# Performance work log

Measured on AMD Instinct MI355X. Metric: run time of the kernel, lower is better.

The kernel has to match this reference:

```python
import jax, jax.numpy as jnp
import numpy as np

N_NODES = 50000
N_EDGES = 600000
IN_DIM = 128
HID = 128


def setup_inputs() -> dict:
    key = jax.random.key(0)
    ks = jax.random.split(key, 8)
    x = jax.random.normal(ks[0], (N_NODES, IN_DIM), dtype=jnp.float32)
    edge_index = jax.random.randint(ks[1], (2, N_EDGES), 0, N_NODES, dtype=jnp.int64)
    def lin(k, fan_in, fan_out):
        s = 1.0 / np.sqrt(fan_in)
        kw, kb = jax.random.split(k)
        W = jax.random.uniform(kw, (fan_in, fan_out), jnp.float32, -s, s)
        b = jax.random.uniform(kb, (fan_out,), jnp.float32, -s, s)
        return W, b
    W0, b0 = lin(ks[2], IN_DIM, HID)
    W1, b1 = lin(ks[3], HID, HID)
    W2, b2 = lin(ks[4], HID, HID)
    return {"x": x, "edge_index": edge_index, "W0": W0, "b0": b0,
            "W1": W1, "b1": b1, "W2": W2, "b2": b2}


def reference(x, edge_index, W0, b0, W1, b1, W2, b2):
    n = x.shape[0]
    loops = jnp.arange(n, dtype=edge_index.dtype)
    src = jnp.concatenate([edge_index[0], loops])  # source nodes (+self loops)
    dst = jnp.concatenate([edge_index[1], loops])  # destination nodes
    # symmetric GCN normalization: deg^{-1/2}[src] * deg^{-1/2}[dst]
    deg = jax.ops.segment_sum(jnp.ones(src.shape[0], x.dtype), dst, num_segments=n)
    dinv = jnp.where(deg > 0, jax.lax.rsqrt(deg), 0.0)
    norm = dinv[src] * dinv[dst]  # [E+N]

    def gcn_layer(h, W, b):
        hw = h @ W                              # [N, H]
        msg = hw[src] * norm[:, None]           # gather + scale, [E+N, H]
        agg = jax.ops.segment_sum(msg, dst, num_segments=n)  # scatter-add
        return agg + b

    h = x
    for W, b in ((W0, b0), (W1, b1), (W2, b2)):
        h = jax.nn.relu(gcn_layer(h, W, b))     # dropout is identity in eval
    return h  # JK='last'
```

## Files before the change

### kernel.cpp

```cpp
#include <hip/hip_runtime.h>

#define NN 50000
#define NE 600000
#define DIM 128
#define NB_N 196
#define NB_E 2344
#define TILES 3125
#define ROWW 136
#define NEPAD (NE + 16 * NN + 64)

#define B_PAD 196
#define B_SENT (NB_E + B_PAD)
#define B_GEMM0 (B_SENT + 1)
#define NB_GEMM 782
#define NB_FILL (B_GEMM0 + NB_GEMM)

typedef unsigned short u16;
typedef unsigned int u32;
typedef __attribute__((ext_vector_type(8))) short bf16x8;
typedef __attribute__((ext_vector_type(4))) float f32x4;

__device__ __forceinline__ u16 f2bf(float f) {
    u32 u = __builtin_bit_cast(u32, f);
    u32 r = (u + 0x7FFFu + ((u >> 16) & 1u)) >> 16;
    return (u16)r;
}
__device__ __forceinline__ float bflo(u32 w) { return __builtin_bit_cast(float, w << 16); }
__device__ __forceinline__ float bfhi(u32 w) { return __builtin_bit_cast(float, w & 0xffff0000u); }
__device__ __forceinline__ int pad16(int d) {
    int p = (d + 15) & ~15;
    return p < 16 ? 16 : p;
}

__global__ __launch_bounds__(256) void k_count(const int* __restrict__ ei,
                                               int* __restrict__ deg,
                                               int* __restrict__ rank,
                                               const float* __restrict__ W0,
                                               const float* __restrict__ W1,
                                               const float* __restrict__ W2,
                                               u16* __restrict__ Wt) {
    int b = blockIdx.x;
    if (b >= NB_E) {
        int idx = (b - NB_E) * 256 + threadIdx.x;
        int l = idx >> 14, rem = idx & 16383;
        int n = rem >> 7, k = rem & 127;
        const float* W = (l == 0) ? W0 : ((l == 1) ? W1 : W2);
        Wt[idx] = f2bf(W[k * 128 + n]);
        return;
    }
    __shared__ int s64;
    if (threadIdx.x == 0) {
        int o = 0;
#pragma unroll
        for (int j = 0; j < 16; j++) o |= ei[2 * j + 1];
        s64 = (o == 0);
    }
    __syncthreads();
    int e = b * 256 + threadIdx.x;
    if (e >= NE) return;
    int d = s64 ? ei[2 * (NE + e)] : ei[NE + e];
    rank[e] = atomicAdd(&deg[d], 1);
}

__global__ __launch_bounds__(256) void k_scanA(const int* __restrict__ deg,
                                               int* __restrict__ rp8,
                                               int* __restrict__ bsum) {
    __shared__ int buf[256];
    int t = threadIdx.x, i = blockIdx.x * 256 + t;
    int v = (i < NN) ? pad16(deg[i]) : 0;
    buf[t] = v;
    __syncthreads();
    for (int off = 1; off < 256; off <<= 1) {
        int x = (t >= off) ? buf[t - off] : 0;
        __syncthreads();
        buf[t] += x;
        __syncthreads();
    }
    if (i < NN) rp8[i] = buf[t] - v;
    if (t == 255) bsum[blockIdx.x] = buf[255];
}

__global__ __launch_bounds__(256) void k_scanB(int* __restrict__ bsum) {
    __shared__ int buf[256];
    int t = threadIdx.x;
    int v = (t < NB_N) ? bsum[t] : 0;
    buf[t] = v;
    __syncthreads();
    for (int off = 1; off < 256; off <<= 1) {
        int x = (t >= off) ? buf[t - off] : 0;
        __syncthreads();
        buf[t] += x;
        __syncthreads();
    }
    bsum[t] = buf[t] - v;
}

__global__ __launch_bounds__(256) void k_scanC(const int* __restrict__ deg,
                                               int* __restrict__ rp8,
                                               const int* __restrict__ bsum,
                                               float* __restrict__ dinv) {
    int i = blockIdx.x * 256 + threadIdx.x;
    if (i < NN) {
        rp8[i] += bsum[i >> 8];
        dinv[i] = rsqrtf((float)(deg[i] + 1));
    }
    if (i == 0) rp8[NN] = bsum[255];
}

__global__ __launch_bounds__(256) void k_fill(const int* __restrict__ ei,
                                              const int* __restrict__ rp8,
                                              const int* __restrict__ rank,
                                              const int* __restrict__ deg,
                                              int* __restrict__ recs,
                                              const float* __restrict__ x,
                                              const u16* __restrict__ Wt,
                                              const float* __restrict__ dinv,
                                              u16* __restrict__ hwA,
                                              u16* __restrict__ hwB) {
    int b = blockIdx.x;
    if (b < NB_E) {
        __shared__ int s64;
        if (threadIdx.x == 0) {
            int o = 0;
#pragma unroll
            for (int j = 0; j < 16; j++) o |= ei[2 * j + 1];
            s64 = (o == 0);
        }
        __syncthreads();
        int e = b * 256 + threadIdx.x;
        if (e >= NE) return;
        int is64 = s64;
        int s = is64 ? ei[2 * e] : ei[e];
        int d = is64 ? ei[2 * (NE + e)] : ei[NE + e];
        recs[rp8[d] + rank[e]] = s;
        return;
    }
    if (b < B_SENT) {
        int i = (b - NB_E) * 256 + threadIdx.x;
        if (i < NN) {
            int rp = rp8[i], d = deg[i], p = pad16(d);
            for (int j = d; j < p; j++) recs[rp + j] = NN;
        }
        return;
    }
    if (b == B_SENT) {
        if (threadIdx.x < 64) {
            ((u32*)(hwA + (size_t)NN * DIM))[threadIdx.x] = 0;
            ((u32*)(hwB + (size_t)NN * DIM))[threadIdx.x] = 0;
        }
        return;
    }
    int lane = threadIdx.x & 63;
    int tile = (b - B_GEMM0) * 4 + (threadIdx.x >> 6);
    if (tile >= TILES) return;
    int r = lane & 15, q = lane >> 4;
    long rowbase = (long)tile * 16;
    bf16x8 Af[4];
#pragma unroll
    for (int kc = 0; kc < 4; kc++) {
        const float4* p = (const float4*)(x + (rowbase + r) * 128 + kc * 32 + q * 8);
        float4 t0 = p[0], t1 = p[1];
        bf16x8 a;
        a[0] = (short)f2bf(t0.x); a[1] = (short)f2bf(t0.y);
        a[2] = (short)f2bf(t0.z); a[3] = (short)f2bf(t0.w);
        a[4] = (short)f2bf(t1.x); a[5] = (short)f2bf(t1.y);
        a[6] = (short)f2bf(t1.z); a[7] = (short)f2bf(t1.w);
        Af[kc] = a;
    }
    float dv[4];
#pragma unroll
    for (int i = 0; i < 4; i++) dv[i] = dinv[rowbase + q * 4 + i];
#pragma unroll
    for (int nt = 0; nt < 8; nt++) {
        f32x4 acc = {0.f, 0.f, 0.f, 0.f};
#pragma unroll
        for (int kc = 0; kc < 4; kc++) {
            bf16x8 Bf = *(const bf16x8*)(Wt + ((nt * 16 + r) << 7) + kc * 32 + q * 8);
            acc = __builtin_amdgcn_mfma_f32_16x16x32_bf16(Af[kc], Bf, acc, 0, 0, 0);
        }
#pragma unroll
        for (int i = 0; i < 4; i++)
            hwA[(rowbase + q * 4 + i) * 128 + nt * 16 + r] = f2bf(dv[i] * acc[i]);
    }
}

__device__ __forceinline__ void add8(float* a, uint4 u) {
    a[0] += bflo(u.x); a[1] += bfhi(u.x);
    a[2] += bflo(u.y); a[3] += bfhi(u.y);
    a[4] += bflo(u.z); a[5] += bfhi(u.z);
    a[6] += bflo(u.w); a[7] += bfhi(u.w);
}

__device__ __forceinline__ void agg_pair(const u16* __restrict__ hw,
                                         const int* __restrict__ rp8,
                                         const int* __restrict__ recs,
                                         int va, int vb, int g, int r,
                                         float* A, float* B) {
    uint4 sva = *(const uint4*)(hw + (size_t)va * DIM + r * 8);
    uint4 svb = *(const uint4*)(hw + (size_t)vb * DIM + r * 8);
    float m = (g == 0) ? 1.0f : 0.0f;
    A[0] = m * bflo(sva.x); A[1] = m * bfhi(sva.x);
    A[2] = m * bflo(sva.y); A[3] = m * bfhi(sva.y);
    A[4] = m * bflo(sva.z); A[5] = m * bfhi(sva.z);
    A[6] = m * bflo(sva.w); A[7] = m * bfhi(sva.w);
    B[0] = m * bflo(svb.x); B[1] = m * bfhi(svb.x);
    B[2] = m * bflo(svb.y); B[3] = m * bfhi(svb.y);
    B[4] = m * bflo(svb.z); B[5] = m * bfhi(svb.z);
    B[6] = m * bflo(svb.w); B[7] = m * bfhi(svb.w);

    int ea = rp8[va], enda = rp8[va + 1];
    int eb = rp8[vb], endb = rp8[vb + 1];
    const int go = 4 * g;
    int4 qa = *(const int4*)(recs + ea + go);
    int4 qb = *(const int4*)(recs + eb + go);
    while (ea < enda || eb < endb) {
        int sa0 = (ea < enda) ? qa.x : NN;
        int sa1 = (ea < enda) ? qa.y : NN;
        int sa2 = (ea < enda) ? qa.z : NN;
        int sa3 = (ea < enda) ? qa.w : NN;
        int sb0 = (eb < endb) ? qb.x : NN;
        int sb1 = (eb < endb) ? qb.y : NN;
        int sb2 = (eb < endb) ? qb.z : NN;
        int sb3 = (eb < endb) ? qb.w : NN;
        uint4 ua0 = *(const uint4*)(hw + (size_t)(u32)sa0 * DIM + r * 8);
        uint4 ua1 = *(const uint4*)(hw + (size_t)(u32)sa1 * DIM + r * 8);
        uint4 ua2 = *(const uint4*)(hw + (size_t)(u32)sa2 * DIM + r * 8);
        uint4 ua3 = *(const uint4*)(hw + (size_t)(u32)sa3 * DIM + r * 8);
        uint4 ub0 = *(const uint4*)(hw + (size_t)(u32)sb0 * DIM + r * 8);
        uint4 ub1 = *(const uint4*)(hw + (size_t)(u32)sb1 * DIM + r * 8);
        uint4 ub2 = *(const uint4*)(hw + (size_t)(u32)sb2 * DIM + r * 8);
        uint4 ub3 = *(const uint4*)(hw + (size_t)(u32)sb3 * DIM + r * 8);
        ea += 16; eb += 16;
        int4 qa_n = *(const int4*)(recs + min(ea, enda - 16) + go);
        int4 qb_n = *(const int4*)(recs + min(eb, endb - 16) + go);
        add8(A, ua0); add8(A, ua1); add8(A, ua2); add8(A, ua3);
        add8(B, ub0); add8(B, ub1); add8(B, ub2); add8(B, ub3);
        qa = qa_n; qb = qb_n;
    }
}

__device__ __forceinline__ void combine_scale(float dv, const float* bias, int r,
                                              float* acc) {
#pragma unroll
    for (int j = 0; j < 8; j++) {
        acc[j] += __shfl_xor(acc[j], 16, 64);
        acc[j] += __shfl_xor(acc[j], 32, 64);
    }
    float4 b0 = ((const float4*)bias)[2 * r];
    float4 b1 = ((const float4*)bias)[2 * r + 1];
    acc[0] = fmaxf(fmaf(dv, acc[0], b0.x), 0.f);
    acc[1] = fmaxf(fmaf(dv, acc[1], b0.y), 0.f);
    acc[2] = fmaxf(fmaf(dv, acc[2], b0.z), 0.f);
    acc[3] = fmaxf(fmaf(dv, acc[3], b0.w), 0.f);
    acc[4] = fmaxf(fmaf(dv, acc[4], b1.x), 0.f);
    acc[5] = fmaxf(fmaf(dv, acc[5], b1.y), 0.f);
    acc[6] = fmaxf(fmaf(dv, acc[6], b1.z), 0.f);
    acc[7] = fmaxf(fmaf(dv, acc[7], b1.w), 0.f);
}

__global__ __launch_bounds__(256) void k_agg_gemm(const u16* __restrict__ hw_in,
                                                  const int* __restrict__ rp8,
                                                  const int* __restrict__ recs,
                                                  const float* __restrict__ dinv,
                                                  const float* __restrict__ bias,
                                                  const u16* __restrict__ Wt,
                                                  u16* __restrict__ hw_out) {
    __shared__ u16 sm[16 * ROWW];
    int lane = threadIdx.x & 63;
    int w = threadIdx.x >> 6;
    int g = lane >> 4, r = lane & 15;
    int base = blockIdx.x * 16;
#pragma unroll
    for (int p = 0; p < 2; p++) {
        int rowa = w * 4 + 2 * p;
        int va = base + rowa;
        float A[8], B[8];
        agg_pair(hw_in, rp8, recs, va, va + 1, g, r, A, B);
        combine_scale(dinv[va], bias, r, A);
        combine_scale(dinv[va + 1], bias, r, B);
        if (g == 0) {
            uint4 pk;
            pk.x = (u32)f2bf(A[0]) | ((u32)f2bf(A[1]) << 16);
            pk.y = (u32)f2bf(A[2]) | ((u32)f2bf(A[3]) << 16);
            pk.z = (u32)f2bf(A[4]) | ((u32)f2bf(A[5]) << 16);
            pk.w = (u32)f2bf(A[6]) | ((u32)f2bf(A[7]) << 16);
            *(uint4*)(sm + rowa * ROWW + r * 8) = pk;
            pk.x = (u32)f2bf(B[0]) | ((u32)f2bf(B[1]) << 16);
            pk.y = (u32)f2bf(B[2]) | ((u32)f2bf(B[3]) << 16);
            pk.z = (u32)f2bf(B[4]) | ((u32)f2bf(B[5]) << 16);
            pk.w = (u32)f2bf(B[6]) | ((u32)f2bf(B[7]) << 16);
            *(uint4*)(sm + (rowa + 1) * ROWW + r * 8) = pk;
        }
    }
    __syncthreads();
    int q = lane >> 4;
    bf16x8 Af[4];
#pragma unroll
    for (int kc = 0; kc < 4; kc++)
        Af[kc] = *(const bf16x8*)(sm + r * ROWW + kc * 32 + q * 8);
    float dv[4];
#pragma unroll
    for (int i = 0; i < 4; i++) dv[i] = dinv[base + q * 4 + i];
#pragma unroll
    for (int t = 0; t < 2; t++) {
        int nt = w * 2 + t;
        f32x4 acc = {0.f, 0.f, 0.f, 0.f};
#pragma unroll
        for (int kc = 0; kc < 4; kc++) {
            bf16x8 Bf = *(const bf16x8*)(Wt + ((nt * 16 + r) << 7) + kc * 32 + q * 8);
            acc = __builtin_amdgcn_mfma_f32_16x16x32_bf16(Af[kc], Bf, acc, 0, 0, 0);
        }
#pragma unroll
        for (int i = 0; i < 4; i++)
            hw_out[(size_t)(base + q * 4 + i) * DIM + nt * 16 + r] = f2bf(dv[i] * acc[i]);
    }
}

__global__ __launch_bounds__(256) void k_agg_out(const u16* __restrict__ hw_in,
                                                 const int* __restrict__ rp8,
                                                 const int* __restrict__ recs,
                                                 const float* __restrict__ dinv,
                                                 const float* __restrict__ bias,
                                                 float* __restrict__ out) {
    int lane = threadIdx.x & 63;
    int w = threadIdx.x >> 6;
    int g = lane >> 4, r = lane & 15;
    int va = blockIdx.x * 8 + w * 2;
    float A[8], B[8];
    agg_pair(hw_in, rp8, recs, va, va + 1, g, r, A, B);
    combine_scale(dinv[va], bias, r, A);
    combine_scale(dinv[va + 1], bias, r, B);
    if (g == 0) {
        float4* p = (float4*)(out + (size_t)va * DIM + r * 8);
        p[0] = make_float4(A[0], A[1], A[2], A[3]);
        p[1] = make_float4(A[4], A[5], A[6], A[7]);
        p = (float4*)(out + (size_t)(va + 1) * DIM + r * 8);
        p[0] = make_float4(B[0], B[1], B[2], B[3]);
        p[1] = make_float4(B[4], B[5], B[6], B[7]);
    }
}


extern "C" void kernel_launch(void* const* d_in, const int* in_sizes, int n_in,
                              void* d_out, int out_size, void* d_ws, size_t ws_size,
                              hipStream_t stream) {
    const float* x = (const float*)d_in[0];
    const int* ei = (const int*)d_in[1];
    const float* W0 = (const float*)d_in[2];
    const float* b0 = (const float*)d_in[3];
    const float* W1 = (const float*)d_in[4];
    const float* b1 = (const float*)d_in[5];
    const float* W2 = (const float*)d_in[6];
    const float* b2 = (const float*)d_in[7];

    char* ws = (char*)d_ws;
    size_t off = 0;
    auto alloc = [&](size_t bytes) -> void* {
        void* p = ws + off;
        off += (bytes + 511) & ~(size_t)511;
        return p;
    };
    int* deg = (int*)alloc(NN * 4);
    size_t zbytes = off;
    int* rank = (int*)alloc((size_t)NE * 4);
    int* recs = (int*)alloc((size_t)NEPAD * 4);
    float* dinv = (float*)alloc(NN * 4);
    int* rp8 = (int*)alloc((NN + 1) * 4);
    int* bsum = (int*)alloc(256 * 4);
    u16* Wt = (u16*)alloc(3 * 128 * 128 * 2);
    u16* hwA = (u16*)alloc((size_t)(NN + 1) * DIM * 2);
    u16* hwB = (u16*)alloc((size_t)(NN + 1) * DIM * 2);

    hipMemsetAsync(ws, 0, zbytes, stream);
    k_count<<<NB_E + 192, 256, 0, stream>>>(ei, deg, rank, W0, W1, W2, Wt);
    k_scanA<<<NB_N, 256, 0, stream>>>(deg, rp8, bsum);
    k_scanB<<<1, 256, 0, stream>>>(bsum);
    k_scanC<<<NB_N, 256, 0, stream>>>(deg, rp8, bsum, dinv);
    k_fill<<<NB_FILL, 256, 0, stream>>>(ei, rp8, rank, deg, recs, x, Wt, dinv,
                                        hwA, hwB);
    k_agg_gemm<<<TILES, 256, 0, stream>>>(hwA, rp8, recs, dinv, b0,
                                          Wt + 16384, hwB);
    k_agg_gemm<<<TILES, 256, 0, stream>>>(hwB, rp8, recs, dinv, b1,
                                          Wt + 32768, hwA);
    k_agg_out<<<6250, 256, 0, stream>>>(hwA, rp8, recs, dinv, b2,
                                        (float*)d_out);
}
```

Measured before the change: 245.1 us.

## Aggregate four nodes per wavefront and merge scan passes into fewer launches

The gather-aggregate routine now handles four destination nodes per wavefront instead of two. It issues the neighbor-index and row loads for all four up front to expose more memory-level parallelism, and uses packed float2 accumulation. The edge count and fill kernels now process two edges per thread with vector loads. The separate block-sum scan kernel is removed: each k_scanC block recomputes its own prefix with a wave reduction. The wider per-wave work raises register pressure and load imbalance between the four nodes' degree loops.

```diff
diff --git a/kernel.cpp b/kernel.cpp
--- a/kernel.cpp
+++ b/kernel.cpp
@@ -4,13 +4,13 @@
 #define NE 600000
 #define DIM 128
 #define NB_N 196
-#define NB_E 2344
+#define NB_E2 1172
 #define TILES 3125
 #define ROWW 136
 #define NEPAD (NE + 16 * NN + 64)
 
-#define B_PAD 196
-#define B_SENT (NB_E + B_PAD)
+#define B_PAD NB_N
+#define B_SENT (NB_E2 + B_PAD)
 #define B_GEMM0 (B_SENT + 1)
 #define NB_GEMM 782
 #define NB_FILL (B_GEMM0 + NB_GEMM)
@@ -19,6 +19,7 @@
 typedef unsigned int u32;
 typedef __attribute__((ext_vector_type(8))) short bf16x8;
 typedef __attribute__((ext_vector_type(4))) float f32x4;
+typedef __attribute__((ext_vector_type(2))) float f32x2;
 
 __device__ __forceinline__ u16 f2bf(float f) {
     u32 u = __builtin_bit_cast(u32, f);
@@ -27,6 +28,9 @@
 }
 __device__ __forceinline__ float bflo(u32 w) { return __builtin_bit_cast(float, w << 16); }
 __device__ __forceinline__ float bfhi(u32 w) { return __builtin_bit_cast(float, w & 0xffff0000u); }
+__device__ __forceinline__ f32x2 unp(u32 w) {
+    f32x2 v; v.x = bflo(w); v.y = bfhi(w); return v;
+}
 __device__ __forceinline__ int pad16(int d) {
     int p = (d + 15) & ~15;
     return p < 16 ? 16 : p;
@@ -40,8 +44,8 @@
                                                const float* __restrict__ W2,
                                                u16* __restrict__ Wt) {
     int b = blockIdx.x;
-    if (b >= NB_E) {
-        int idx = (b - NB_E) * 256 + threadIdx.x;
+    if (b >= NB_E2) {
+        int idx = (b - NB_E2) * 256 + threadIdx.x;
         int l = idx >> 14, rem = idx & 16383;
         int n = rem >> 7, k = rem & 127;
         const float* W = (l == 0) ? W0 : ((l == 1) ? W1 : W2);
@@ -56,10 +60,20 @@
         s64 = (o == 0);
     }
     __syncthreads();
-    int e = b * 256 + threadIdx.x;
-    if (e >= NE) return;
-    int d = s64 ? ei[2 * (NE + e)] : ei[NE + e];
-    rank[e] = atomicAdd(&deg[d], 1);
+    int p = b * 256 + threadIdx.x;
+    int ebase = 2 * p;
+    if (ebase >= NE) return;
+    int d0, d1;
+    if (s64) {
+        int4 dd = *(const int4*)(ei + 2 * (NE + ebase));
+        d0 = dd.x; d1 = dd.z;
+    } else {
+        int2 dd = *(const int2*)(ei + NE + ebase);
+        d0 = dd.x; d1 = dd.y;
+    }
+    int r0 = atomicAdd(&deg[d0], 1);
+    int r1 = atomicAdd(&deg[d1], 1);
+    *(int2*)(rank + ebase) = make_int2(r0, r1);
 }
 
 __global__ __launch_bounds__(256) void k_scanA(const int* __restrict__ deg,
@@ -80,31 +94,31 @@
     if (t == 255) bsum[blockIdx.x] = buf[255];
 }
 
-__global__ __launch_bounds__(256) void k_scanB(int* __restrict__ bsum) {
-    __shared__ int buf[256];
-    int t = threadIdx.x;
-    int v = (t < NB_N) ? bsum[t] : 0;
-    buf[t] = v;
-    __syncthreads();
-    for (int off = 1; off < 256; off <<= 1) {
-        int x = (t >= off) ? buf[t - off] : 0;
-        __syncthreads();
-        buf[t] += x;
-        __syncthreads();
-    }
-    bsum[t] = buf[t] - v;
-}
-
 __global__ __launch_bounds__(256) void k_scanC(const int* __restrict__ deg,
                                                int* __restrict__ rp8,
                                                const int* __restrict__ bsum,
                                                float* __restrict__ dinv) {
+    __shared__ int soff, stot;
+    if (threadIdx.x < 64) {
+        int accP = 0, accT = 0;
+        for (int j = threadIdx.x; j < NB_N; j += 64) {
+            int v = bsum[j];
+            accT += v;
+            if (j < (int)blockIdx.x) accP += v;
+        }
+        for (int off = 1; off < 64; off <<= 1) {
+            accP += __shfl_xor(accP, off, 64);
+            accT += __shfl_xor(accT, off, 64);
+        }
+        if (threadIdx.x == 0) { soff = accP; stot = accT; }
+    }
+    __syncthreads();
     int i = blockIdx.x * 256 + threadIdx.x;
     if (i < NN) {
-        rp8[i] += bsum[i >> 8];
+        rp8[i] += soff;
         dinv[i] = rsqrtf((float)(deg[i] + 1));
     }
-    if (i == 0) rp8[NN] = bsum[255];
+    if (i == 0) rp8[NN] = stot;
 }
 
 __global__ __launch_bounds__(256) void k_fill(const int* __restrict__ ei,
@@ -118,7 +132,7 @@
                                               u16* __restrict__ hwA,
                                               u16* __restrict__ hwB) {
     int b = blockIdx.x;
-    if (b < NB_E) {
+    if (b < NB_E2) {
         __shared__ int s64;
         if (threadIdx.x == 0) {
             int o = 0;
@@ -127,16 +141,26 @@
             s64 = (o == 0);
         }
         __syncthreads();
-        int e = b * 256 + threadIdx.x;
-        if (e >= NE) return;
-        int is64 = s64;
-        int s = is64 ? ei[2 * e] : ei[e];
-        int d = is64 ? ei[2 * (NE + e)] : ei[NE + e];
-        recs[rp8[d] + rank[e]] = s;
+        int p = b * 256 + threadIdx.x;
+        int ebase = 2 * p;
+        if (ebase >= NE) return;
+        int s0, s1, d0, d1;
+        if (s64) {
+            int4 ss = *(const int4*)(ei + 2 * ebase);
+            int4 dd = *(const int4*)(ei + 2 * (NE + ebase));
+            s0 = ss.x; s1 = ss.z; d0 = dd.x; d1 = dd.z;
+        } else {
+            int2 ss = *(const int2*)(ei + ebase);
+            int2 dd = *(const int2*)(ei + NE + ebase);
+            s0 = ss.x; s1 = ss.y; d0 = dd.x; d1 = dd.y;
+        }
+        int2 rk = *(const int2*)(rank + ebase);
+        recs[rp8[d0] + rk.x] = s0;
+        recs[rp8[d1] + rk.y] = s1;
         return;
     }
     if (b < B_SENT) {
-        int i = (b - NB_E) * 256 + threadIdx.x;
+        int i = (b - NB_E2) * 256 + threadIdx.x;
         if (i < NN) {
             int rp = rp8[i], d = deg[i], p = pad16(d);
             for (int j = d; j < p; j++) recs[rp + j] = NN;
@@ -184,78 +208,116 @@
     }
 }
 
-__device__ __forceinline__ void add8(float* a, uint4 u) {
-    a[0] += bflo(u.x); a[1] += bfhi(u.x);
-    a[2] += bflo(u.y); a[3] += bfhi(u.y);
-    a[4] += bflo(u.z); a[5] += bfhi(u.z);
-    a[6] += bflo(u.w); a[7] += bfhi(u.w);
-}
-
-__device__ __forceinline__ void agg_pair(const u16* __restrict__ hw,
+__device__ __forceinline__ void acc8(f32x2* a, uint4 u) {
+    a[0] += unp(u.x); a[1] += unp(u.y); a[2] += unp(u.z); a[3] += unp(u.w);
+}
+
+__device__ __forceinline__ uint4 ldrow(const u16* __restrict__ hw, int s, int r) {
+    return *(const uint4*)(hw + (size_t)(u32)s * DIM + r * 8);
+}
+
+__device__ __forceinline__ void agg_quad(const u16* __restrict__ hw,
                                          const int* __restrict__ rp8,
                                          const int* __restrict__ recs,
-                                         int va, int vb, int g, int r,
-                                         float* A, float* B) {
-    uint4 sva = *(const uint4*)(hw + (size_t)va * DIM + r * 8);
-    uint4 svb = *(const uint4*)(hw + (size_t)vb * DIM + r * 8);
+                                         int v0, int g, int r,
+                                         f32x2* A0, f32x2* A1, f32x2* A2, f32x2* A3) {
+    int4 rr = *(const int4*)(rp8 + v0);
+    int n3 = rp8[v0 + 4];
+    int e0 = rr.x, e1 = rr.y, e2 = rr.z, e3 = rr.w;
+    int n0 = e1, n1 = e2, n2 = e3;
+    const int go = 4 * g;
+    int4 q0 = *(const int4*)(recs + e0 + go);
+    int4 q1 = *(const int4*)(recs + e1 + go);
+    int4 q2 = *(const int4*)(recs + e2 + go);
+    int4 q3 = *(const int4*)(recs + e3 + go);
+    uint4 s0 = ldrow(hw, v0, r);
+    uint4 s1 = ldrow(hw, v0 + 1, r);
+    uint4 s2 = ldrow(hw, v0 + 2, r);
+    uint4 s3 = ldrow(hw, v0 + 3, r);
     float m = (g == 0) ? 1.0f : 0.0f;
-    A[0] = m * bflo(sva.x); A[1] = m * bfhi(sva.x);
-    A[2] = m * bflo(sva.y); A[3] = m * bfhi(sva.y);
-    A[4] = m * bflo(sva.z); A[5] = m * bfhi(sva.z);
-    A[6] = m * bflo(sva.w); A[7] = m * bfhi(sva.w);
-    B[0] = m * bflo(svb.x); B[1] = m * bfhi(svb.x);
-    B[2] = m * bflo(svb.y); B[3] = m * bfhi(svb.y);
-    B[4] = m * bflo(svb.z); B[5] = m * bfhi(svb.z);
-    B[6] = m * bflo(svb.w); B[7] = m * bfhi(svb.w);
-
-    int ea = rp8[va], enda = rp8[va + 1];
-    int eb = rp8[vb], endb = rp8[vb + 1];
-    const int go = 4 * g;
-    int4 qa = *(const int4*)(recs + ea + go);
-    int4 qb = *(const int4*)(recs + eb + go);
-    while (ea < enda || eb < endb) {
-        int sa0 = (ea < enda) ? qa.x : NN;
-        int sa1 = (ea < enda) ? qa.y : NN;
-        int sa2 = (ea < enda) ? qa.z : NN;
-        int sa3 = (ea < enda) ? qa.w : NN;
-        int sb0 = (eb < endb) ? qb.x : NN;
-        int sb1 = (eb < endb) ? qb.y : NN;
-        int sb2 = (eb < endb) ? qb.z : NN;
-        int sb3 = (eb < endb) ? qb.w : NN;
-        uint4 ua0 = *(const uint4*)(hw + (size_t)(u32)sa0 * DIM + r * 8);
-        uint4 ua1 = *(const uint4*)(hw + (size_t)(u32)sa1 * DIM + r * 8);
-        uint4 ua2 = *(const uint4*)(hw + (size_t)(u32)sa2 * DIM + r * 8);
-        uint4 ua3 = *(const uint4*)(hw + (size_t)(u32)sa3 * DIM + r * 8);
-        uint4 ub0 = *(const uint4*)(hw + (size_t)(u32)sb0 * DIM + r * 8);
-        uint4 ub1 = *(const uint4*)(hw + (size_t)(u32)sb1 * DIM + r * 8);
-        uint4 ub2 = *(const uint4*)(hw + (size_t)(u32)sb2 * DIM + r * 8);
-        uint4 ub3 = *(const uint4*)(hw + (size_t)(u32)sb3 * DIM + r * 8);
-        ea += 16; eb += 16;
-        int4 qa_n = *(const int4*)(recs + min(ea, enda - 16) + go);
-        int4 qb_n = *(const int4*)(recs + min(eb, endb - 16) + go);
-        add8(A, ua0); add8(A, ua1); add8(A, ua2); add8(A, ua3);
-        add8(B, ub0); add8(B, ub1); add8(B, ub2); add8(B, ub3);
-        qa = qa_n; qb = qb_n;
-    }
-}
-
-__device__ __forceinline__ void combine_scale(float dv, const float* bias, int r,
-                                              float* acc) {
-#pragma unroll
-    for (int j = 0; j < 8; j++) {
-        acc[j] += __shfl_xor(acc[j], 16, 64);
-        acc[j] += __shfl_xor(acc[j], 32, 64);
+    A0[0] = m * unp(s0.x); A0[1] = m * unp(s0.y); A0[2] = m * unp(s0.z); A0[3] = m * unp(s0.w);
+    A1[0] = m * unp(s1.x); A1[1] = m * unp(s1.y); A1[2] = m * unp(s1.z); A1[3] = m * unp(s1.w);
+    A2[0] = m * unp(s2.x); A2[1] = m * unp(s2.y); A2[2] = m * unp(s2.z); A2[3] = m * unp(s2.w);
+    A3[0] = m * unp(s3.x); A3[1] = m * unp(s3.y); A3[2] = m * unp(s3.z); A3[3] = m * unp(s3.w);
+
+    uint4 u00 = ldrow(hw, q0.x, r), u01 = ldrow(hw, q0.y, r);
+    uint4 u02 = ldrow(hw, q0.z, r), u03 = ldrow(hw, q0.w, r);
+    uint4 u10 = ldrow(hw, q1.x, r), u11 = ldrow(hw, q1.y, r);
+    uint4 u12 = ldrow(hw, q1.z, r), u13 = ldrow(hw, q1.w, r);
+    e0 += 16; e1 += 16; e2 += 16; e3 += 16;
+    acc8(A0, u00); acc8(A0, u01); acc8(A0, u02); acc8(A0, u03);
+    uint4 u20 = ldrow(hw, q2.x, r), u21 = ldrow(hw, q2.y, r);
+    uint4 u22 = ldrow(hw, q2.z, r), u23 = ldrow(hw, q2.w, r);
+    acc8(A1, u10); acc8(A1, u11); acc8(A1, u12); acc8(A1, u13);
+    uint4 u30 = ldrow(hw, q3.x, r), u31 = ldrow(hw, q3.y, r);
+    uint4 u32_ = ldrow(hw, q3.z, r), u33 = ldrow(hw, q3.w, r);
+    q0 = *(const int4*)(recs + min(e0, n0 - 16) + go);
+    q1 = *(const int4*)(recs + min(e1, n1 - 16) + go);
+    q2 = *(const int4*)(recs + min(e2, n2 - 16) + go);
+    q3 = *(const int4*)(recs + min(e3, n3 - 16) + go);
+    acc8(A2, u20); acc8(A2, u21); acc8(A2, u22); acc8(A2, u23);
+    acc8(A3, u30); acc8(A3, u31); acc8(A3, u32_); acc8(A3, u33);
+
+    while ((e0 < n0) | (e1 < n1) | (e2 < n2) | (e3 < n3)) {
+        if (e0 < n0) {
+            uint4 a = ldrow(hw, q0.x, r), b = ldrow(hw, q0.y, r);
+            uint4 c = ldrow(hw, q0.z, r), d = ldrow(hw, q0.w, r);
+            e0 += 16;
+            q0 = *(const int4*)(recs + min(e0, n0 - 16) + go);
+            acc8(A0, a); acc8(A0, b); acc8(A0, c); acc8(A0, d);
+        }
+        if (e1 < n1) {
+            uint4 a = ldrow(hw, q1.x, r), b = ldrow(hw, q1.y, r);
+            uint4 c = ldrow(hw, q1.z, r), d = ldrow(hw, q1.w, r);
+            e1 += 16;
+            q1 = *(const int4*)(recs + min(e1, n1 - 16) + go);
+            acc8(A1, a); acc8(A1, b); acc8(A1, c); acc8(A1, d);
+        }
+        if (e2 < n2) {
+            uint4 a = ldrow(hw, q2.x, r), b = ldrow(hw, q2.y, r);
+            uint4 c = ldrow(hw, q2.z, r), d = ldrow(hw, q2.w, r);
+            e2 += 16;
+            q2 = *(const int4*)(recs + min(e2, n2 - 16) + go);
+            acc8(A2, a); acc8(A2, b); acc8(A2, c); acc8(A2, d);
+        }
+        if (e3 < n3) {
+            uint4 a = ldrow(hw, q3.x, r), b = ldrow(hw, q3.y, r);
+            uint4 c = ldrow(hw, q3.z, r), d = ldrow(hw, q3.w, r);
+            e3 += 16;
+            q3 = *(const int4*)(recs + min(e3, n3 - 16) + go);
+            acc8(A3, a); acc8(A3, b); acc8(A3, c); acc8(A3, d);
+        }
+    }
+}
+
+__device__ __forceinline__ void combine_scale2(float dv, const float* bias, int r,
+                                               f32x2* acc) {
+#pragma unroll
+    for (int j = 0; j < 4; j++) {
+        acc[j].x += __shfl_xor(acc[j].x, 16, 64);
+        acc[j].y += __shfl_xor(acc[j].y, 16, 64);
+        acc[j].x += __shfl_xor(acc[j].x, 32, 64);
+        acc[j].y += __shfl_xor(acc[j].y, 32, 64);
     }
     float4 b0 = ((const float4*)bias)[2 * r];
     float4 b1 = ((const float4*)bias)[2 * r + 1];
-    acc[0] = fmaxf(fmaf(dv, acc[0], b0.x), 0.f);
-    acc[1] = fmaxf(fmaf(dv, acc[1], b0.y), 0.f);
-    acc[2] = fmaxf(fmaf(dv, acc[2], b0.z), 0.f);
-    acc[3] = fmaxf(fmaf(dv, acc[3], b0.w), 0.f);
-    acc[4] = fmaxf(fmaf(dv, acc[4], b1.x), 0.f);
-    acc[5] = fmaxf(fmaf(dv, acc[5], b1.y), 0.f);
-    acc[6] = fmaxf(fmaf(dv, acc[6], b1.z), 0.f);
-    acc[7] = fmaxf(fmaf(dv, acc[7], b1.w), 0.f);
+    acc[0].x = fmaxf(fmaf(dv, acc[0].x, b0.x), 0.f);
+    acc[0].y = fmaxf(fmaf(dv, acc[0].y, b0.y), 0.f);
+    acc[1].x = fmaxf(fmaf(dv, acc[1].x, b0.z), 0.f);
+    acc[1].y = fmaxf(fmaf(dv, acc[1].y, b0.w), 0.f);
+    acc[2].x = fmaxf(fmaf(dv, acc[2].x, b1.x), 0.f);
+    acc[2].y = fmaxf(fmaf(dv, acc[2].y, b1.y), 0.f);
+    acc[3].x = fmaxf(fmaf(dv, acc[3].x, b1.z), 0.f);
+    acc[3].y = fmaxf(fmaf(dv, acc[3].y, b1.w), 0.f);
+}
+
+__device__ __forceinline__ uint4 pk8(const f32x2* A) {
+    uint4 p;
+    p.x = (u32)f2bf(A[0].x) | ((u32)f2bf(A[0].y) << 16);
+    p.y = (u32)f2bf(A[1].x) | ((u32)f2bf(A[1].y) << 16);
+    p.z = (u32)f2bf(A[2].x) | ((u32)f2bf(A[2].y) << 16);
+    p.w = (u32)f2bf(A[3].x) | ((u32)f2bf(A[3].y) << 16);
+    return p;
 }
 
 __global__ __launch_bounds__(256) void k_agg_gemm(const u16* __restrict__ hw_in,
@@ -270,27 +332,20 @@
     int w = threadIdx.x >> 6;
     int g = lane >> 4, r = lane & 15;
     int base = blockIdx.x * 16;
-#pragma unroll
-    for (int p = 0; p < 2; p++) {
-        int rowa = w * 4 + 2 * p;
-        int va = base + rowa;
-        float A[8], B[8];
-        agg_pair(hw_in, rp8, recs, va, va + 1, g, r, A, B);
-        combine_scale(dinv[va], bias, r, A);
-        combine_scale(dinv[va + 1], bias, r, B);
-        if (g == 0) {
-            uint4 pk;
-            pk.x = (u32)f2bf(A[0]) | ((u32)f2bf(A[1]) << 16);
-            pk.y = (u32)f2bf(A[2]) | ((u32)f2bf(A[3]) << 16);
-            pk.z = (u32)f2bf(A[4]) | ((u32)f2bf(A[5]) << 16);
-            pk.w = (u32)f2bf(A[6]) | ((u32)f2bf(A[7]) << 16);
-            *(uint4*)(sm + rowa * ROWW + r * 8) = pk;
-            pk.x = (u32)f2bf(B[0]) | ((u32)f2bf(B[1]) << 16);
-            pk.y = (u32)f2bf(B[2]) | ((u32)f2bf(B[3]) << 16);
-            pk.z = (u32)f2bf(B[4]) | ((u32)f2bf(B[5]) << 16);
-            pk.w = (u32)f2bf(B[6]) | ((u32)f2bf(B[7]) << 16);
-            *(uint4*)(sm + (rowa + 1) * ROWW + r * 8) = pk;
-        }
+    int v0 = base + w * 4;
+    f32x2 A0[4], A1[4], A2[4], A3[4];
+    agg_quad(hw_in, rp8, recs, v0, g, r, A0, A1, A2, A3);
+    float4 dvq = *(const float4*)(dinv + v0);
+    combine_scale2(dvq.x, bias, r, A0);
+    combine_scale2(dvq.y, bias, r, A1);
+    combine_scale2(dvq.z, bias, r, A2);
+    combine_scale2(dvq.w, bias, r, A3);
+    if (g == 0) {
+        int rowa = w * 4;
+        *(uint4*)(sm + (rowa + 0) * ROWW + r * 8) = pk8(A0);
+        *(uint4*)(sm + (rowa + 1) * ROWW + r * 8) = pk8(A1);
+        *(uint4*)(sm + (rowa + 2) * ROWW + r * 8) = pk8(A2);
+        *(uint4*)(sm + (rowa + 3) * ROWW + r * 8) = pk8(A3);
     }
     __syncthreads();
     int q = lane >> 4;
@@ -325,18 +380,22 @@
     int lane = threadIdx.x & 63;
     int w = threadIdx.x >> 6;
     int g = lane >> 4, r = lane & 15;
-    int va = blockIdx.x * 8 + w * 2;
-    float A[8], B[8];
-    agg_pair(hw_in, rp8, recs, va, va + 1, g, r, A, B);
-    combine_scale(dinv[va], bias, r, A);
-    combine_scale(dinv[va + 1], bias, r, B);
+    int v0 = blockIdx.x * 16 + w * 4;
+    f32x2 A0[4], A1[4], A2[4], A3[4];
+    agg_quad(hw_in, rp8, recs, v0, g, r, A0, A1, A2, A3);
+    float4 dvq = *(const float4*)(dinv + v0);
+    combine_scale2(dvq.x, bias, r, A0);
+    combine_scale2(dvq.y, bias, r, A1);
+    combine_scale2(dvq.z, bias, r, A2);
+    combine_scale2(dvq.w, bias, r, A3);
     if (g == 0) {
-        float4* p = (float4*)(out + (size_t)va * DIM + r * 8);
-        p[0] = make_float4(A[0], A[1], A[2], A[3]);
-        p[1] = make_float4(A[4], A[5], A[6], A[7]);
-        p = (float4*)(out + (size_t)(va + 1) * DIM + r * 8);
-        p[0] = make_float4(B[0], B[1], B[2], B[3]);
-        p[1] = make_float4(B[4], B[5], B[6], B[7]);
+        f32x2* a[4] = {A0, A1, A2, A3};
+#pragma unroll
+        for (int i = 0; i < 4; i++) {
+            float4* p = (float4*)(out + (size_t)(v0 + i) * DIM + r * 8);
+            p[0] = make_float4(a[i][0].x, a[i][0].y, a[i][1].x, a[i][1].y);
+            p[1] = make_float4(a[i][2].x, a[i][2].y, a[i][3].x, a[i][3].y);
+        }
     }
 }
 
@@ -365,16 +424,15 @@
     int* rank = (int*)alloc((size_t)NE * 4);
     int* recs = (int*)alloc((size_t)NEPAD * 4);
     float* dinv = (float*)alloc(NN * 4);
-    int* rp8 = (int*)alloc((NN + 1) * 4);
+    int* rp8 = (int*)alloc((NN + 8) * 4);
     int* bsum = (int*)alloc(256 * 4);
     u16* Wt = (u16*)alloc(3 * 128 * 128 * 2);
     u16* hwA = (u16*)alloc((size_t)(NN + 1) * DIM * 2);
     u16* hwB = (u16*)alloc((size_t)(NN + 1) * DIM * 2);
 
     hipMemsetAsync(ws, 0, zbytes, stream);
-    k_count<<<NB_E + 192, 256, 0, stream>>>(ei, deg, rank, W0, W1, W2, Wt);
+    k_count<<<NB_E2 + 192, 256, 0, stream>>>(ei, deg, rank, W0, W1, W2, Wt);
     k_scanA<<<NB_N, 256, 0, stream>>>(deg, rp8, bsum);
-    k_scanB<<<1, 256, 0, stream>>>(bsum);
     k_scanC<<<NB_N, 256, 0, stream>>>(deg, rp8, bsum, dinv);
     k_fill<<<NB_FILL, 256, 0, stream>>>(ei, rp8, rank, deg, recs, x, Wt, dinv,
                                         hwA, hwB);
@@ -382,6 +440,6 @@
                                           Wt + 16384, hwB);
     k_agg_gemm<<<TILES, 256, 0, stream>>>(hwB, rp8, recs, dinv, b1,
                                           Wt + 32768, hwA);
-    k_agg_out<<<6250, 256, 0, stream>>>(hwA, rp8, recs, dinv, b2,
+    k_agg_out<<<3125, 256, 0, stream>>>(hwA, rp8, recs, dinv, b2,
                                         (float*)d_out);
 }
```

New measurement: 249.2 us. No clear change (+1.6%).

## Move layer-0 GEMM into count kernel, fold scanB into scanC, pair edges

Applied to the files above, without the earlier changes.

The layer-0 X@W0 GEMM now runs inside the degree-count kernel, using W0 converted into LDS per block, and writes unscaled fp32 results to a new buffer. A later pass in the scan kernel applies the dinv scaling and converts to bf16. The separate single-block scanB launch is removed, and each scanC block computes its own prefix offset with wave shuffles. Each thread in the count and fill kernels now handles two edges with vector loads. This cuts the number of kernel launches and lets the GEMM overlap with the atomics, at the cost of an extra 25MB fp32 write and read and a per-block conversion of W0 into LDS.

```diff
diff --git a/kernel.cpp b/kernel.cpp
--- a/kernel.cpp
+++ b/kernel.cpp
@@ -4,16 +4,23 @@
 #define NE 600000
 #define DIM 128
 #define NB_N 196
-#define NB_E 2344
+#define NB_E2 1172
 #define TILES 3125
 #define ROWW 136
+#define WPITCH 136
 #define NEPAD (NE + 16 * NN + 64)
 
-#define B_PAD 196
-#define B_SENT (NB_E + B_PAD)
-#define B_GEMM0 (B_SENT + 1)
+#define CB_CAST0 NB_E2
+#define CB_GEMM0 (NB_E2 + 128)
 #define NB_GEMM 782
-#define NB_FILL (B_GEMM0 + NB_GEMM)
+#define NB_CNT (CB_GEMM0 + NB_GEMM)
+
+#define SC_SENT NB_N
+#define SC_SCALE0 (NB_N + 1)
+#define NB_SCALE 6250
+#define NB_SCANC (SC_SCALE0 + NB_SCALE)
+
+#define NB_FILL (NB_E2 + NB_N)
 
 typedef unsigned short u16;
 typedef unsigned int u32;
@@ -38,28 +45,80 @@
                                                const float* __restrict__ W0,
                                                const float* __restrict__ W1,
                                                const float* __restrict__ W2,
-                                               u16* __restrict__ Wt) {
+                                               u16* __restrict__ Wt,
+                                               const float* __restrict__ x,
+                                               float* __restrict__ hF) {
+    __shared__ u16 ldsW[128 * WPITCH];
     int b = blockIdx.x;
-    if (b >= NB_E) {
-        int idx = (b - NB_E) * 256 + threadIdx.x;
+    if (b < NB_E2) {
+        __shared__ int s64;
+        if (threadIdx.x == 0) {
+            int o = 0;
+#pragma unroll
+            for (int j = 0; j < 16; j++) o |= ei[2 * j + 1];
+            s64 = (o == 0);
+        }
+        __syncthreads();
+        int p = b * 256 + threadIdx.x;
+        int ebase = 2 * p;
+        if (ebase >= NE) return;
+        int d0, d1;
+        if (s64) {
+            int4 dd = *(const int4*)(ei + 2 * (NE + ebase));
+            d0 = dd.x; d1 = dd.z;
+        } else {
+            int2 dd = *(const int2*)(ei + NE + ebase);
+            d0 = dd.x; d1 = dd.y;
+        }
+        int r0 = atomicAdd(&deg[d0], 1);
+        int r1 = atomicAdd(&deg[d1], 1);
+        *(int2*)(rank + ebase) = make_int2(r0, r1);
+        return;
+    }
+    if (b < CB_GEMM0) {
+        int idx = (b - CB_CAST0) * 256 + threadIdx.x;
         int l = idx >> 14, rem = idx & 16383;
         int n = rem >> 7, k = rem & 127;
-        const float* W = (l == 0) ? W0 : ((l == 1) ? W1 : W2);
-        Wt[idx] = f2bf(W[k * 128 + n]);
+        const float* W = (l == 0) ? W1 : W2;
+        Wt[16384 + idx] = f2bf(W[k * 128 + n]);
         return;
     }
-    __shared__ int s64;
-    if (threadIdx.x == 0) {
-        int o = 0;
-#pragma unroll
-        for (int j = 0; j < 16; j++) o |= ei[2 * j + 1];
-        s64 = (o == 0);
+    int gb = b - CB_GEMM0;
+    for (int i = 0; i < 64; i++) {
+        int j = i * 256 + threadIdx.x;
+        int k = j >> 7, n = j & 127;
+        ldsW[n * WPITCH + k] = f2bf(W0[j]);
     }
     __syncthreads();
-    int e = b * 256 + threadIdx.x;
-    if (e >= NE) return;
-    int d = s64 ? ei[2 * (NE + e)] : ei[NE + e];
-    rank[e] = atomicAdd(&deg[d], 1);
+    int lane = threadIdx.x & 63;
+    int tile = gb * 4 + (threadIdx.x >> 6);
+    if (tile >= TILES) return;
+    int r = lane & 15, q = lane >> 4;
+    long rowbase = (long)tile * 16;
+    bf16x8 Af[4];
+#pragma unroll
+    for (int kc = 0; kc < 4; kc++) {
+        const float4* p = (const float4*)(x + (rowbase + r) * 128 + kc * 32 + q * 8);
+        float4 t0 = p[0], t1 = p[1];
+        bf16x8 a;
+        a[0] = (short)f2bf(t0.x); a[1] = (short)f2bf(t0.y);
+        a[2] = (short)f2bf(t0.z); a[3] = (short)f2bf(t0.w);
+        a[4] = (short)f2bf(t1.x); a[5] = (short)f2bf(t1.y);
+        a[6] = (short)f2bf(t1.z); a[7] = (short)f2bf(t1.w);
+        Af[kc] = a;
+    }
+#pragma unroll
+    for (int nt = 0; nt < 8; nt++) {
+        f32x4 acc = {0.f, 0.f, 0.f, 0.f};
+#pragma unroll
+        for (int kc = 0; kc < 4; kc++) {
+            bf16x8 Bf = *(const bf16x8*)(ldsW + (nt * 16 + r) * WPITCH + kc * 32 + q * 8);
+            acc = __builtin_amdgcn_mfma_f32_16x16x32_bf16(Af[kc], Bf, acc, 0, 0, 0);
+        }
+#pragma unroll
+        for (int i = 0; i < 4; i++)
+            hF[(rowbase + q * 4 + i) * 128 + nt * 16 + r] = acc[i];
+    }
 }
 
 __global__ __launch_bounds__(256) void k_scanA(const int* __restrict__ deg,
@@ -80,45 +139,62 @@
     if (t == 255) bsum[blockIdx.x] = buf[255];
 }
 
-__global__ __launch_bounds__(256) void k_scanB(int* __restrict__ bsum) {
-    __shared__ int buf[256];
-    int t = threadIdx.x;
-    int v = (t < NB_N) ? bsum[t] : 0;
-    buf[t] = v;
-    __syncthreads();
-    for (int off = 1; off < 256; off <<= 1) {
-        int x = (t >= off) ? buf[t - off] : 0;
-        __syncthreads();
-        buf[t] += x;
-        __syncthreads();
-    }
-    bsum[t] = buf[t] - v;
-}
-
 __global__ __launch_bounds__(256) void k_scanC(const int* __restrict__ deg,
                                                int* __restrict__ rp8,
                                                const int* __restrict__ bsum,
-                                               float* __restrict__ dinv) {
-    int i = blockIdx.x * 256 + threadIdx.x;
-    if (i < NN) {
-        rp8[i] += bsum[i >> 8];
-        dinv[i] = rsqrtf((float)(deg[i] + 1));
-    }
-    if (i == 0) rp8[NN] = bsum[255];
+                                               float* __restrict__ dinv,
+                                               const float* __restrict__ hF,
+                                               u16* __restrict__ hwA,
+                                               u16* __restrict__ hwB) {
+    int b = blockIdx.x;
+    if (b < NB_N) {
+        __shared__ int soff, stot;
+        if (threadIdx.x < 64) {
+            int accP = 0, accT = 0;
+            for (int j = threadIdx.x; j < NB_N; j += 64) {
+                int v = bsum[j];
+                accT += v;
+                if (j < b) accP += v;
+            }
+            for (int off = 1; off < 64; off <<= 1) {
+                accP += __shfl_xor(accP, off, 64);
+                accT += __shfl_xor(accT, off, 64);
+            }
+            if (threadIdx.x == 0) { soff = accP; stot = accT; }
+        }
+        __syncthreads();
+        int i = b * 256 + threadIdx.x;
+        if (i < NN) {
+            rp8[i] += soff;
+            dinv[i] = rsqrtf((float)(deg[i] + 1));
+        }
+        if (i == 0) rp8[NN] = stot;
+        return;
+    }
+    if (b == SC_SENT) {
+        if (threadIdx.x < 64) {
+            ((u32*)(hwA + (size_t)NN * DIM))[threadIdx.x] = 0;
+        } else if (threadIdx.x < 128) {
+            ((u32*)(hwB + (size_t)NN * DIM))[threadIdx.x - 64] = 0;
+        }
+        return;
+    }
+    int idx = (b - SC_SCALE0) * 256 + threadIdx.x;
+    int row = idx >> 5, part = idx & 31;
+    float dv = rsqrtf((float)(deg[row] + 1));
+    float4 v = *(const float4*)(hF + (size_t)row * 128 + part * 4);
+    u32 lo = (u32)f2bf(dv * v.x) | ((u32)f2bf(dv * v.y) << 16);
+    u32 hi = (u32)f2bf(dv * v.z) | ((u32)f2bf(dv * v.w) << 16);
+    *(uint2*)(hwA + (size_t)row * 128 + part * 4) = make_uint2(lo, hi);
 }
 
 __global__ __launch_bounds__(256) void k_fill(const int* __restrict__ ei,
                                               const int* __restrict__ rp8,
                                               const int* __restrict__ rank,
                                               const int* __restrict__ deg,
-                                              int* __restrict__ recs,
-                                              const float* __restrict__ x,
-                                              const u16* __restrict__ Wt,
-                                              const float* __restrict__ dinv,
-                                              u16* __restrict__ hwA,
-                                              u16* __restrict__ hwB) {
+                                              int* __restrict__ recs) {
     int b = blockIdx.x;
-    if (b < NB_E) {
+    if (b < NB_E2) {
         __shared__ int s64;
         if (threadIdx.x == 0) {
             int o = 0;
@@ -127,60 +203,28 @@
             s64 = (o == 0);
         }
         __syncthreads();
-        int e = b * 256 + threadIdx.x;
-        if (e >= NE) return;
-        int is64 = s64;
-        int s = is64 ? ei[2 * e] : ei[e];
-        int d = is64 ? ei[2 * (NE + e)] : ei[NE + e];
-        recs[rp8[d] + rank[e]] = s;
+        int p = b * 256 + threadIdx.x;
+        int ebase = 2 * p;
+        if (ebase >= NE) return;
+        int s0, s1, d0, d1;
+        if (s64) {
+            int4 ss = *(const int4*)(ei + 2 * ebase);
+            int4 dd = *(const int4*)(ei + 2 * (NE + ebase));
+            s0 = ss.x; s1 = ss.z; d0 = dd.x; d1 = dd.z;
+        } else {
+            int2 ss = *(const int2*)(ei + ebase);
+            int2 dd = *(const int2*)(ei + NE + ebase);
+            s0 = ss.x; s1 = ss.y; d0 = dd.x; d1 = dd.y;
+        }
+        int2 rk = *(const int2*)(rank + ebase);
+        recs[rp8[d0] + rk.x] = s0;
+        recs[rp8[d1] + rk.y] = s1;
         return;
     }
-    if (b < B_SENT) {
-        int i = (b - NB_E) * 256 + threadIdx.x;
-        if (i < NN) {
-            int rp = rp8[i], d = deg[i], p = pad16(d);
-            for (int j = d; j < p; j++) recs[rp + j] = NN;
-        }
-        return;
-    }
-    if (b == B_SENT) {
-        if (threadIdx.x < 64) {
-            ((u32*)(hwA + (size_t)NN * DIM))[threadIdx.x] = 0;
-            ((u32*)(hwB + (size_t)NN * DIM))[threadIdx.x] = 0;
-        }
-        return;
-    }
-    int lane = threadIdx.x & 63;
-    int tile = (b - B_GEMM0) * 4 + (threadIdx.x >> 6);
-    if (tile >= TILES) return;
-    int r = lane & 15, q = lane >> 4;
-    long rowbase = (long)tile * 16;
-    bf16x8 Af[4];
-#pragma unroll
-    for (int kc = 0; kc < 4; kc++) {
-        const float4* p = (const float4*)(x + (rowbase + r) * 128 + kc * 32 + q * 8);
-        float4 t0 = p[0], t1 = p[1];
-        bf16x8 a;
-        a[0] = (short)f2bf(t0.x); a[1] = (short)f2bf(t0.y);
-        a[2] = (short)f2bf(t0.z); a[3] = (short)f2bf(t0.w);
-        a[4] = (short)f2bf(t1.x); a[5] = (short)f2bf(t1.y);
-        a[6] = (short)f2bf(t1.z); a[7] = (short)f2bf(t1.w);
-        Af[kc] = a;
-    }
-    float dv[4];
-#pragma unroll
-    for (int i = 0; i < 4; i++) dv[i] = dinv[rowbase + q * 4 + i];
-#pragma unroll
-    for (int nt = 0; nt < 8; nt++) {
-        f32x4 acc = {0.f, 0.f, 0.f, 0.f};
-#pragma unroll
-        for (int kc = 0; kc < 4; kc++) {
-            bf16x8 Bf = *(const bf16x8*)(Wt + ((nt * 16 + r) << 7) + kc * 32 + q * 8);
-            acc = __builtin_amdgcn_mfma_f32_16x16x32_bf16(Af[kc], Bf, acc, 0, 0, 0);
-        }
-#pragma unroll
-        for (int i = 0; i < 4; i++)
-            hwA[(rowbase + q * 4 + i) * 128 + nt * 16 + r] = f2bf(dv[i] * acc[i]);
+    int i = (b - NB_E2) * 256 + threadIdx.x;
+    if (i < NN) {
+        int rp = rp8[i], d = deg[i], p = pad16(d);
+        for (int j = d; j < p; j++) recs[rp + j] = NN;
     }
 }
 
@@ -365,19 +409,18 @@
     int* rank = (int*)alloc((size_t)NE * 4);
     int* recs = (int*)alloc((size_t)NEPAD * 4);
     float* dinv = (float*)alloc(NN * 4);
-    int* rp8 = (int*)alloc((NN + 1) * 4);
+    int* rp8 = (int*)alloc((NN + 8) * 4);
     int* bsum = (int*)alloc(256 * 4);
     u16* Wt = (u16*)alloc(3 * 128 * 128 * 2);
     u16* hwA = (u16*)alloc((size_t)(NN + 1) * DIM * 2);
     u16* hwB = (u16*)alloc((size_t)(NN + 1) * DIM * 2);
+    float* hF = (float*)alloc((size_t)NN * DIM * 4);
 
     hipMemsetAsync(ws, 0, zbytes, stream);
-    k_count<<<NB_E + 192, 256, 0, stream>>>(ei, deg, rank, W0, W1, W2, Wt);
+    k_count<<<NB_CNT, 256, 0, stream>>>(ei, deg, rank, W0, W1, W2, Wt, x, hF);
     k_scanA<<<NB_N, 256, 0, stream>>>(deg, rp8, bsum);
-    k_scanB<<<1, 256, 0, stream>>>(bsum);
-    k_scanC<<<NB_N, 256, 0, stream>>>(deg, rp8, bsum, dinv);
-    k_fill<<<NB_FILL, 256, 0, stream>>>(ei, rp8, rank, deg, recs, x, Wt, dinv,
-                                        hwA, hwB);
+    k_scanC<<<NB_SCANC, 256, 0, stream>>>(deg, rp8, bsum, dinv, hF, hwA, hwB);
+    k_fill<<<NB_FILL, 256, 0, stream>>>(ei, rp8, rank, deg, recs);
     k_agg_gemm<<<TILES, 256, 0, stream>>>(hwA, rp8, recs, dinv, b0,
                                           Wt + 16384, hwB);
     k_agg_gemm<<<TILES, 256, 0, stream>>>(hwB, rp8, recs, dinv, b1,
```

After: 238.4 us. -2.8%, faster.
